# Optimization experiments

Measured on AMD Instinct MI355X. Metric: run time of the kernel, lower is better.

Reference implementation:

```python
import jax, jax.numpy as jnp
import numpy as np

EPS = 1e-5

def gather_neighbour(pc, idx):
    # pc: [B,N,d], idx: [B,Q,k] -> [B,Q,k,d]
    return jax.vmap(lambda p, i: p[i])(pc, idx)

def rel_pos_encoding(q_xyz, src_xyz, idx):
    # q_xyz: [B,Q,3], src_xyz: [B,N,3], idx: [B,Q,k] -> [B,Q,k,10]
    nbr = gather_neighbour(src_xyz, idx)              # [B,Q,k,3]
    tile = q_xyz[:, :, None, :]                       # [B,Q,1,3]
    rel = tile - nbr                                  # [B,Q,k,3]
    dis = jnp.sqrt(jnp.sum(rel * rel, axis=-1, keepdims=True))
    tile_b = jnp.broadcast_to(tile, nbr.shape)
    return jnp.concatenate([dis, rel, tile_b, nbr], axis=-1)

def conv_bn_relu(x, W, g, b, m, v):
    # 1x1 conv (bias-free) + inference BatchNorm + ReLU; x: [B,Q,K,Cin], W: [Cout,Cin]
    y = jnp.einsum('bqkc,oc->bqko', x, W)
    y = (y - m) * (g * jax.lax.rsqrt(v + EPS)) + b
    return jax.nn.relu(y)

def att_pool(x, Wfc, Wm, g, b, m, v):
    # x: [B,Q,K,C] -> [B,Q,1,Cout]; softmax over neighbor axis K
    att = jnp.einsum('bqkc,oc->bqko', x, Wfc)
    att = jax.nn.softmax(att, axis=2)
    agg = jnp.sum(x * att, axis=2, keepdims=True)     # [B,Q,1,C]
    return conv_bn_relu(agg, Wm, g, b, m, v)

def setup_inputs() -> dict:
    key = jax.random.key(0)
    ks = jax.random.split(key, 40)
    B, Q, k, Nd, Ns = 2, 16384, 16, 4096, 16384
    dim_lb, dim_sc, dim_nl = 128, 64, 128
    d_mid = dim_lb + 10 - dim_sc   # 74
    d_att = dim_lb + 10            # 138
    f32 = jnp.float32
    inp = {}
    inp['features_lb'] = jax.random.normal(ks[0], (B, Q, k, dim_lb), f32)
    inp['features_sc'] = jax.random.normal(ks[1], (B, Q, k, dim_sc), f32)
    inp['NM_lb'] = jax.random.randint(ks[2], (B, Q, k), 0, Nd)
    inp['NM_sc'] = jax.random.randint(ks[3], (B, Q, k), 0, Ns)
    inp['coords_lb'] = jax.random.normal(ks[4], (B, Nd, 3), f32)
    inp['coords_sc'] = jax.random.normal(ks[5], (B, Ns, 3), f32)
    inp['coords_queries'] = jax.random.normal(ks[6], (B, Q, 3), f32)
    inp['NM_cl'] = jax.random.randint(ks[7], (B, Q, k), 0, Q)
    def bn(i, c):
        return (jax.random.uniform(ks[i], (c,), f32) + 0.5,
                jax.random.normal(ks[i + 1], (c,), f32) * 0.1,
                jax.random.normal(ks[i + 2], (c,), f32) * 0.1,
                jax.random.uniform(ks[i + 3], (c,), f32) + 0.5)
    inp['W_lb'] = jax.random.normal(ks[8], (10, 10), f32) * 0.3
    inp['g_lb'], inp['b_lb'], inp['m_lb'], inp['v_lb'] = bn(9, 10)
    inp['W_sc'] = jax.random.normal(ks[13], (d_mid, 10), f32) * 0.3
    inp['g_sc'], inp['b_sc'], inp['m_sc'], inp['v_sc'] = bn(14, d_mid)
    inp['W_fc1'] = jax.random.normal(ks[18], (d_att, d_att), f32) * 0.08
    inp['W_mlp1'] = jax.random.normal(ks[19], (dim_nl, d_att), f32) * 0.08
    inp['g1'], inp['b1'], inp['m1'], inp['v1'] = bn(20, dim_nl)
    inp['W_cl'] = jax.random.normal(ks[24], (10, 10), f32) * 0.3
    inp['g_cl'], inp['b_cl'], inp['m_cl'], inp['v_cl'] = bn(25, 10)
    inp['W_fc2'] = jax.random.normal(ks[29], (d_att, d_att), f32) * 0.08
    inp['W_mlp2'] = jax.random.normal(ks[30], (dim_nl, d_att), f32) * 0.08
    inp['g2'], inp['b2'], inp['m2'], inp['v2'] = bn(31, dim_nl)
    return inp

def reference(features_lb, features_sc, NM_lb, NM_sc, coords_lb, coords_sc,
              coords_queries, NM_cl,
              W_lb, g_lb, b_lb, m_lb, v_lb,
              W_sc, g_sc, b_sc, m_sc, v_sc,
              W_fc1, W_mlp1, g1, b1, m1, v1,
              W_cl, g_cl, b_cl, m_cl, v_cl,
              W_fc2, W_mlp2, g2, b2, m2, v2):
    # branch 1: layer-below
    rppe_lb = conv_bn_relu(rel_pos_encoding(coords_queries, coords_lb, NM_lb),
                           W_lb, g_lb, b_lb, m_lb, v_lb)          # [B,Q,k,10]
    # branch 2: skip connection
    rppe_sc = conv_bn_relu(rel_pos_encoding(coords_queries, coords_sc, NM_sc),
                           W_sc, g_sc, b_sc, m_sc, v_sc)          # [B,Q,k,74]
    locSE_lb = jnp.concatenate([rppe_lb, features_lb], axis=-1)   # [B,Q,k,138]
    locSE_sc = jnp.concatenate([rppe_sc, features_sc], axis=-1)   # [B,Q,k,138]
    f_hat = jnp.concatenate([locSE_lb, locSE_sc], axis=2)         # [B,Q,2k,138]
    f_tilde = att_pool(f_hat, W_fc1, W_mlp1, g1, b1, m1, v1)      # [B,Q,1,128]
    # second aggregation over current layer (num_agg > 1)
    rppe_cl = conv_bn_relu(rel_pos_encoding(coords_queries, coords_queries, NM_cl),
                           W_cl, g_cl, b_cl, m_cl, v_cl)          # [B,Q,k,10]
    f_cur = gather_neighbour(f_tilde[:, :, 0, :], NM_cl)          # [B,Q,k,128]
    locSE_cl = jnp.concatenate([rppe_cl, f_cur], axis=-1)         # [B,Q,k,138]
    f_tilde = att_pool(locSE_cl, W_fc2, W_mlp2, g2, b2, m2, v2)   # [B,Q,1,128]
    # match torch output layout [B, dim_nl, Q, 1]
    return jnp.transpose(f_tilde, (0, 3, 1, 2))
```

## Files before the change

kernel.cpp:

```cpp
#include <hip/hip_runtime.h>
#include <cmath>

#define EPSF 1e-5f
typedef unsigned int  uint32;
typedef unsigned short u16;
typedef __attribute__((ext_vector_type(8))) short bfrag;
typedef __attribute__((ext_vector_type(4))) float f32x4;

constexpr int Qn   = 16384;
constexpr int KS   = 168;
constexpr int PXS  = 42;
constexpr int AGS  = 168;
constexpr int Nd   = 4096;
constexpr float LOG2E = 1.4426950408889634f;

constexpr int OFF_W1  = 0;
constexpr int OFF_WM1 = 23040;
constexpr int OFF_W2  = 43520;
constexpr int OFF_WM2 = 66560;
constexpr int OFF_WLB = 87040;
constexpr int OFF_WSC = 87552;
constexpr int OFF_WCL = 90112;
constexpr int END_W   = 90624;
constexpr int BN_LB = 0;
constexpr int BN_SC = 20;
constexpr int BN_CL = 168;
constexpr int BN_M1 = 188;
constexpr int BN_M2 = 444;
constexpr int BN_TOT = 700;
constexpr int OFF_FT  = END_W + 2 * BN_TOT;
constexpr int PREP_N  = END_W + BN_TOT;

__device__ __forceinline__ u16 f2b(float f) {
    uint32 u = __float_as_uint(f);
    uint32 r = (u + 0x7fffu + ((u >> 16) & 1u)) >> 16;
    return (u16)r;
}
__device__ __forceinline__ float b2f(u16 h) {
    return __uint_as_float(((uint32)h) << 16);
}
__device__ __forceinline__ uint32 cvtpk(float a, float b) {
    uint32 r;
    asm("v_cvt_pk_bf16_f32 %0, %1, %2" : "=v"(r) : "v"(a), "v"(b));
    return r;
}
__device__ __forceinline__ u16 cvt1(float a) { return (u16)cvtpk(a, a); }
__device__ __forceinline__ float exp2_hw(float x) { return __builtin_amdgcn_exp2f(x); }

__global__ __launch_bounds__(256) void prep_weights(
    const float* __restrict__ Wfc1, const float* __restrict__ Wmlp1,
    const float* __restrict__ Wfc2, const float* __restrict__ Wmlp2,
    const float* __restrict__ Wlb,  const float* __restrict__ Wsc,
    const float* __restrict__ Wcl,
    const float* __restrict__ g_lb, const float* __restrict__ b_lb,
    const float* __restrict__ m_lb, const float* __restrict__ v_lb,
    const float* __restrict__ g_sc, const float* __restrict__ b_sc,
    const float* __restrict__ m_sc, const float* __restrict__ v_sc,
    const float* __restrict__ g_cl, const float* __restrict__ b_cl,
    const float* __restrict__ m_cl, const float* __restrict__ v_cl,
    const float* __restrict__ g1, const float* __restrict__ b1,
    const float* __restrict__ m1, const float* __restrict__ v1,
    const float* __restrict__ g2, const float* __restrict__ b2,
    const float* __restrict__ m2, const float* __restrict__ v2,
    u16* __restrict__ ws16)
{
    int i = blockIdx.x * 256 + threadIdx.x;
    if (i >= PREP_N) return;
    if (i >= END_W) {
        int j = i - END_W;
        const float *g, *bb, *m, *v; int o2;
        if (j < BN_SC)      { g = g_lb; bb = b_lb; m = m_lb; v = v_lb; o2 = j - BN_LB; }
        else if (j < BN_CL) { g = g_sc; bb = b_sc; m = m_sc; v = v_sc; o2 = j - BN_SC; }
        else if (j < BN_M1) { g = g_cl; bb = b_cl; m = m_cl; v = v_cl; o2 = j - BN_CL; }
        else if (j < BN_M2) { g = g1;   bb = b1;   m = m1;   v = v1;   o2 = j - BN_M1; }
        else                { g = g2;   bb = b2;   m = m2;   v = v2;   o2 = j - BN_M2; }
        int o = o2 >> 1;
        float sc_ = g[o] * rsqrtf(v[o] + EPSF);
        ((float*)(ws16 + END_W))[j] = (o2 & 1) ? (bb[o] - m[o] * sc_) : sc_;
        return;
    }
    int lane = (i >> 3) & 63, jj = i & 7;
    int row16 = lane & 15;
    int kf = ((lane >> 4) << 3) + jj;
    float v = 0.f;
    if (i < OFF_WLB) {
        const float* src; int nrows; int idx; bool fc = false;
        if (i < OFF_WM1)      { src = Wfc1;  nrows = 138; idx = i - OFF_W1;  fc = true; }
        else if (i < OFF_W2)  { src = Wmlp1; nrows = 128; idx = i - OFF_WM1; }
        else if (i < OFF_WM2) { src = Wfc2;  nrows = 138; idx = i - OFF_W2;  fc = true; }
        else                  { src = Wmlp2; nrows = 128; idx = i - OFF_WM2; }
        int t = idx >> 9, nt = t / 5, kt = t - nt * 5;
        int row = nt * 16 + row16;
        int kp  = kt * 32 + kf;
        int k   = (kp < 10) ? kp : kp - 2;
        if (row < nrows && kp < 140 && kp != 10 && kp != 11) {
            v = src[row * 138 + k];
            if (fc) v *= LOG2E;
        }
    } else {
        const float* src; int nrows; int idx;
        if (i < OFF_WSC)      { src = Wlb; nrows = 10; idx = i - OFF_WLB; }
        else if (i < OFF_WCL) { src = Wsc; nrows = 74; idx = i - OFF_WSC; }
        else                  { src = Wcl; nrows = 10; idx = i - OFF_WCL; }
        int t = idx >> 9;
        int row = t * 16 + row16;
        if (row < nrows && kf < 10) v = src[row * 10 + kf];
    }
    ws16[i] = f2b(v);
}

__device__ __forceinline__ void loadB(bfrag (&bf)[5], const u16* __restrict__ Wt,
                                      int nt, int lane) {
    #pragma unroll
    for (int kt = 0; kt < 5; ++kt)
        bf[kt] = *(const bfrag*)&Wt[((nt * 5 + kt) << 9) + (lane << 3)];
}
__device__ __forceinline__ void mfma32(const bfrag (&af)[2][5], const bfrag (&bf)[5],
                                       f32x4 &a0, f32x4 &a1) {
    const f32x4 zf = {0.f, 0.f, 0.f, 0.f};
    a0 = zf; a1 = zf;
    #pragma unroll
    for (int kt = 0; kt < 5; ++kt) {
        a0 = __builtin_amdgcn_mfma_f32_16x16x32_bf16(af[0][kt], bf[kt], a0, 0, 0, 0);
        a1 = __builtin_amdgcn_mfma_f32_16x16x32_bf16(af[1][kt], bf[kt], a1, 0, 0, 0);
    }
}
__device__ __forceinline__ void mfma16(const bfrag (&af)[5], const bfrag (&bf)[5],
                                       f32x4 &a0) {
    const f32x4 zf = {0.f, 0.f, 0.f, 0.f};
    a0 = zf;
    #pragma unroll
    for (int kt = 0; kt < 5; ++kt)
        a0 = __builtin_amdgcn_mfma_f32_16x16x32_bf16(af[kt], bf[kt], a0, 0, 0, 0);
}
__device__ __forceinline__ void soft32(
    const f32x4& a0, const f32x4& a1, int nt,
    int lane, int lrow, const u16* __restrict__ fr0, const u16* __restrict__ fr1,
    u16* __restrict__ ag)
{
    const int ch  = nt * 16 + lrow;
    const int chp = ch + (ch >= 10 ? 2 : 0);
    float s = 0.f, num = 0.f;
    #pragma unroll
    for (int r = 0; r < 4; ++r) {
        float e = exp2_hw(a0[r]);
        s += e;
        num += e * b2f(fr0[r * KS + chp]);
    }
    #pragma unroll
    for (int r = 0; r < 4; ++r) {
        float e = exp2_hw(a1[r]);
        s += e;
        num += e * b2f(fr1[r * KS + chp]);
    }
    s   += __shfl_xor(s, 16);   s   += __shfl_xor(s, 32);
    num += __shfl_xor(num, 16); num += __shfl_xor(num, 32);
    if (lane < 16)
        ag[chp] = cvt1((ch < 138) ? num * __builtin_amdgcn_rcpf(s) : 0.f);
}
__device__ __forceinline__ void soft16(
    const f32x4& a0, int nt,
    int lane, int lrow, const u16* __restrict__ fr0, u16* __restrict__ ag)
{
    const int ch  = nt * 16 + lrow;
    const int chp = ch + (ch >= 10 ? 2 : 0);
    float s = 0.f, num = 0.f;
    #pragma unroll
    for (int r = 0; r < 4; ++r) {
        float e = exp2_hw(a0[r]);
        s += e;
        num += e * b2f(fr0[r * KS + chp]);
    }
    s   += __shfl_xor(s, 16);   s   += __shfl_xor(s, 32);
    num += __shfl_xor(num, 16); num += __shfl_xor(num, 32);
    if (lane < 16)
        ag[chp] = cvt1((ch < 138) ? num * __builtin_amdgcn_rcpf(s) : 0.f);
}
#define SB() __builtin_amdgcn_sched_barrier(0)

__global__ __launch_bounds__(256, 4) void stage1(
    const float* __restrict__ feat_lb, const float* __restrict__ feat_sc,
    const int* __restrict__ nm_lb, const int* __restrict__ nm_sc,
    const float* __restrict__ c_lb, const float* __restrict__ c_sc,
    const float* __restrict__ c_q,
    u16* __restrict__ ws16)
{
    __shared__ __align__(16) u16 fhat[64 * KS];
    __shared__ __align__(16) u16 pxs[64 * PXS];
    u16* aggs = pxs;

    const int tid  = threadIdx.x;
    const int bq0  = blockIdx.x * 2;
    const int b    = bq0 >> 14;
    const int lane = tid & 63;
    const int w    = tid >> 6;
    const int lrow = lane & 15;
    const int lgr  = lane >> 4;
    const int q    = w >> 1;
    const int h    = w & 1;

    const u16* W1t  = ws16 + OFF_W1;
    const u16* Wm1t = ws16 + OFF_WM1;
    const float* bn = (const float*)(ws16 + END_W);
    u16* ft = ws16 + OFF_FT;

    bfrag wcv[3];
    float2 bnv[3];
    if (h == 0) {
        wcv[0] = *(const bfrag*)&ws16[OFF_WLB + (lane << 3)];
        wcv[1] = *(const bfrag*)&ws16[OFF_WSC + (lane << 3)];
        wcv[2] = *(const bfrag*)&ws16[OFF_WSC + 512 + (lane << 3)];
        bnv[0] = (lrow < 10) ? *(const float2*)&bn[BN_LB + lrow * 2] : float2{0.f, 0.f};
        bnv[1] = *(const float2*)&bn[BN_SC + lrow * 2];
        bnv[2] = *(const float2*)&bn[BN_SC + (16 + lrow) * 2];
    } else {
        #pragma unroll
        for (int t = 0; t < 3; ++t) {
            wcv[t] = *(const bfrag*)&ws16[OFF_WSC + ((2 + t) << 9) + (lane << 3)];
            int o = (2 + t) * 16 + lrow;
            bnv[t] = (o < 74) ? *(const float2*)&bn[BN_SC + o * 2] : float2{0.f, 0.f};
        }
    }

    {
        const float4* flb = (const float4*)(feat_lb + (size_t)bq0 * 2048);
        float4 r0[4];
        #pragma unroll
        for (int it = 0; it < 4; ++it) r0[it] = flb[tid + it * 256];
        const float4* fsc = (const float4*)(feat_sc + (size_t)bq0 * 1024);
        float4 r1[2];
        #pragma unroll
        for (int it = 0; it < 2; ++it) r1[it] = fsc[tid + it * 256];
        #pragma unroll
        for (int it = 0; it < 4; ++it) {
            int u = tid + it * 256;
            int qq = u >> 9, rem = u & 511, r = rem >> 5, c4 = rem & 31;
            uint32* d = (uint32*)&fhat[(qq * 32 + r) * KS + 12 + c4 * 4];
            d[0] = cvtpk(r0[it].x, r0[it].y); d[1] = cvtpk(r0[it].z, r0[it].w);
        }
        #pragma unroll
        for (int it = 0; it < 2; ++it) {
            int u = tid + it * 256;
            int qq = u >> 8, rem = u & 255, r = rem >> 4, c4 = rem & 15;
            uint32* d = (uint32*)&fhat[(qq * 32 + 16 + r) * KS + 76 + c4 * 4];
            d[0] = cvtpk(r1[it].x, r1[it].y); d[1] = cvtpk(r1[it].z, r1[it].w);
        }
        for (int u = tid; u < 64 * 15; u += 256) {
            int row = u / 15, jj = u - row * 15;
            uint32* base = (uint32*)((char*)fhat + row * 336);
            if (jj == 0) base[5] = 0u; else base[69 + jj] = 0u;
        }
    }
    if (tid < 64) {
        const int qq = tid >> 5, r = tid & 31;
        const int bq = bq0 + qq;
        const bool lb = r < 16;
        const int idx = lb ? nm_lb[bq * 16 + r] : nm_sc[bq * 16 + (r - 16)];
        const float* nb = lb ? (c_lb + ((size_t)b * Nd + idx) * 3)
                             : (c_sc + ((size_t)b * Qn + idx) * 3);
        const float qx = c_q[bq * 3 + 0], qy = c_q[bq * 3 + 1], qz = c_q[bq * 3 + 2];
        const float nx = nb[0], ny = nb[1], nz = nb[2];
        const float rx = qx - nx, ry = qy - ny, rz = qz - nz;
        const float dd = sqrtf(rx * rx + ry * ry + rz * rz);
        uint32* pw = (uint32*)&pxs[tid * PXS];
        pw[0] = cvtpk(dd, rx); pw[1] = cvtpk(ry, rz); pw[2] = cvtpk(qx, qy);
        pw[3] = cvtpk(qz, nx); pw[4] = cvtpk(ny, nz);
        #pragma unroll
        for (int z = 5; z < 16; ++z) pw[z] = 0u;
    }
    __syncthreads();

    const f32x4 zf = {0.f, 0.f, 0.f, 0.f};

    {
        bfrag pa1 = *(const bfrag*)&pxs[(q * 32 + 16 + lrow) * PXS + lgr * 8];
        if (h == 0) {
            bfrag pa0 = *(const bfrag*)&pxs[(q * 32 + lrow) * PXS + lgr * 8];
            f32x4 c = __builtin_amdgcn_mfma_f32_16x16x32_bf16(pa0, wcv[0], zf, 0, 0, 0);
            if (lrow < 10) {
                #pragma unroll
                for (int r = 0; r < 4; ++r)
                    fhat[(q * 32 + lgr * 4 + r) * KS + lrow] =
                        cvt1(fmaxf(c[r] * bnv[0].x + bnv[0].y, 0.f));
            }
            #pragma unroll
            for (int t = 1; t < 3; ++t) {
                f32x4 c2 = __builtin_amdgcn_mfma_f32_16x16x32_bf16(pa1, wcv[t], zf, 0, 0, 0);
                const int o  = (t - 1) * 16 + lrow;
                const int cp = (o < 10) ? o : o + 2;
                #pragma unroll
                for (int r = 0; r < 4; ++r)
                    fhat[(q * 32 + 16 + lgr * 4 + r) * KS + cp] =
                        cvt1(fmaxf(c2[r] * bnv[t].x + bnv[t].y, 0.f));
            }
        } else {
            #pragma unroll
            for (int t = 0; t < 3; ++t) {
                f32x4 c2 = __builtin_amdgcn_mfma_f32_16x16x32_bf16(pa1, wcv[t], zf, 0, 0, 0);
                const int o = (2 + t) * 16 + lrow;
                if (o < 74) {
                    #pragma unroll
                    for (int r = 0; r < 4; ++r)
                        fhat[(q * 32 + 16 + lgr * 4 + r) * KS + o + 2] =
                            cvt1(fmaxf(c2[r] * bnv[t].x + bnv[t].y, 0.f));
                }
            }
        }
    }
    __syncthreads();

    bfrag af[2][5];
    #pragma unroll
    for (int mt = 0; mt < 2; ++mt)
        #pragma unroll
        for (int kt = 0; kt < 5; ++kt)
            af[mt][kt] = *(const bfrag*)&fhat[(q * 32 + mt * 16 + lrow) * KS + kt * 32 + lgr * 8];

    const u16* fr0 = fhat + (q * 32 + lgr * 4) * KS;
    const u16* fr1 = fr0 + 16 * KS;
    u16* ag = aggs + q * AGS;

    bfrag b0[5], b1[5];
    f32x4 a0, a1;
    if (h == 0) {
        loadB(b0, W1t, 0, lane);
        loadB(b1, W1t, 1, lane); mfma32(af, b0, a0, a1); SB(); soft32(a0, a1, 0, lane, lrow, fr0, fr1, ag);
        loadB(b0, W1t, 2, lane); mfma32(af, b1, a0, a1); SB(); soft32(a0, a1, 1, lane, lrow, fr0, fr1, ag);
        loadB(b1, W1t, 3, lane); mfma32(af, b0, a0, a1); SB(); soft32(a0, a1, 2, lane, lrow, fr0, fr1, ag);
        loadB(b0, W1t, 4, lane); mfma32(af, b1, a0, a1); SB(); soft32(a0, a1, 3, lane, lrow, fr0, fr1, ag);
        mfma32(af, b0, a0, a1); soft32(a0, a1, 4, lane, lrow, fr0, fr1, ag);
        if (lane < 2)       ag[10 + lane] = 0;
        else if (lane < 16) ag[144 + lane] = 0;
    } else {
        loadB(b0, W1t, 5, lane);
        loadB(b1, W1t, 6, lane); mfma32(af, b0, a0, a1); SB(); soft32(a0, a1, 5, lane, lrow, fr0, fr1, ag);
        loadB(b0, W1t, 7, lane); mfma32(af, b1, a0, a1); SB(); soft32(a0, a1, 6, lane, lrow, fr0, fr1, ag);
        loadB(b1, W1t, 8, lane); mfma32(af, b0, a0, a1); SB(); soft32(a0, a1, 7, lane, lrow, fr0, fr1, ag);
        mfma32(af, b1, a0, a1); soft32(a0, a1, 8, lane, lrow, fr0, fr1, ag);
    }
    __syncthreads();

    bfrag am[5];
    #pragma unroll
    for (int kt = 0; kt < 5; ++kt)
        am[kt] = *(const bfrag*)&aggs[lrow * AGS + kt * 32 + lgr * 8];
    #pragma unroll
    for (int oi = 0; oi < 2; ++oi) {
        const int ot = w * 2 + oi;
        f32x4 c = zf;
        #pragma unroll
        for (int kt = 0; kt < 5; ++kt) {
            bfrag wm = *(const bfrag*)&Wm1t[(((ot * 5) + kt) << 9) + (lane << 3)];
            c = __builtin_amdgcn_mfma_f32_16x16x32_bf16(am[kt], wm, c, 0, 0, 0);
        }
        if (lgr == 0) {
            const int o = ot * 16 + lrow;
            float2 p = *(const float2*)&bn[BN_M1 + o * 2];
            #pragma unroll
            for (int r = 0; r < 2; ++r)
                ft[(size_t)(bq0 + r) * 128 + o] = cvt1(fmaxf(c[r] * p.x + p.y, 0.f));
        }
    }
}

__global__ __launch_bounds__(512, 4) void stage2(
    const int* __restrict__ nm_cl, const float* __restrict__ c_q,
    const u16* __restrict__ ws16, float* __restrict__ out)
{
    __shared__ __align__(16) u16 fhat[128 * KS];
    __shared__ __align__(16) u16 pxs[128 * PXS];
    u16* aggs = pxs;

    const int tid  = threadIdx.x;
    const int bq0  = blockIdx.x * 8;
    const int b    = bq0 >> 14;
    const int q0   = bq0 & (Qn - 1);
    const int lane = tid & 63;
    const int w    = tid >> 6;
    const int lrow = lane & 15;
    const int lgr  = lane >> 4;

    const u16* W2t  = ws16 + OFF_W2;
    const u16* Wm2t = ws16 + OFF_WM2;
    const float* bn = (const float*)(ws16 + END_W);
    const u16* ft   = ws16 + OFF_FT;

    bfrag wcl = *(const bfrag*)&ws16[OFF_WCL + (lane << 3)];
    float2 bncl = (lrow < 10) ? *(const float2*)&bn[BN_CL + lrow * 2] : float2{0.f, 0.f};

    for (int u = tid; u < 128 * 15; u += 512) {
        int row = u / 15, jj = u - row * 15;
        uint32* base = (uint32*)((char*)fhat + row * 336);
        if (jj == 0) base[5] = 0u; else base[69 + jj] = 0u;
    }
    if (tid < 128) {
        const int qq = tid >> 4, r = tid & 15;
        const int bq = bq0 + qq;
        const int idx = nm_cl[bq * 16 + r];
        const float* nb = c_q + ((size_t)(b << 14) + idx) * 3;
        const float qx = c_q[bq * 3 + 0], qy = c_q[bq * 3 + 1], qz = c_q[bq * 3 + 2];
        const float nx = nb[0], ny = nb[1], nz = nb[2];
        const float rx = qx - nx, ry = qy - ny, rz = qz - nz;
        const float dd = sqrtf(rx * rx + ry * ry + rz * rz);
        uint32* pw = (uint32*)&pxs[tid * PXS];
        pw[0] = cvtpk(dd, rx); pw[1] = cvtpk(ry, rz); pw[2] = cvtpk(qx, qy);
        pw[3] = cvtpk(qz, nx); pw[4] = cvtpk(ny, nz);
        #pragma unroll
        for (int z = 5; z < 16; ++z) pw[z] = 0u;
    }
    #pragma unroll
    for (int i = 0; i < 16; ++i) {
        int u = tid + i * 512;
        int row = u >> 6, c2 = u & 63;
        int qq = row >> 4;
        int idx = nm_cl[(bq0 + qq) * 16 + (row & 15)];
        const uint32* srow = (const uint32*)(ft + (size_t)((b << 14) + idx) * 128);
        *(uint32*)&fhat[row * KS + 12 + c2 * 2] = srow[c2];
    }
    __syncthreads();

    const f32x4 zf = {0.f, 0.f, 0.f, 0.f};

    {
        bfrag pa = *(const bfrag*)&pxs[(w * 16 + lrow) * PXS + lgr * 8];
        f32x4 c = __builtin_amdgcn_mfma_f32_16x16x32_bf16(pa, wcl, zf, 0, 0, 0);
        if (lrow < 10) {
            #pragma unroll
            for (int r = 0; r < 4; ++r)
                fhat[(w * 16 + lgr * 4 + r) * KS + lrow] =
                    cvt1(fmaxf(c[r] * bncl.x + bncl.y, 0.f));
        }
    }
    __syncthreads();

    bfrag af[5];
    #pragma unroll
    for (int kt = 0; kt < 5; ++kt)
        af[kt] = *(const bfrag*)&fhat[(w * 16 + lrow) * KS + kt * 32 + lgr * 8];

    const u16* fr0 = fhat + (w * 16 + lgr * 4) * KS;
    u16* ag = aggs + w * AGS;

    bfrag b0[5], b1[5];
    f32x4 a0;
    loadB(b0, W2t, 0, lane);
    loadB(b1, W2t, 1, lane); mfma16(af, b0, a0); SB(); soft16(a0, 0, lane, lrow, fr0, ag);
    loadB(b0, W2t, 2, lane); mfma16(af, b1, a0); SB(); soft16(a0, 1, lane, lrow, fr0, ag);
    loadB(b1, W2t, 3, lane); mfma16(af, b0, a0); SB(); soft16(a0, 2, lane, lrow, fr0, ag);
    loadB(b0, W2t, 4, lane); mfma16(af, b1, a0); SB(); soft16(a0, 3, lane, lrow, fr0, ag);
    loadB(b1, W2t, 5, lane); mfma16(af, b0, a0); SB(); soft16(a0, 4, lane, lrow, fr0, ag);
    loadB(b0, W2t, 6, lane); mfma16(af, b1, a0); SB(); soft16(a0, 5, lane, lrow, fr0, ag);
    loadB(b1, W2t, 7, lane); mfma16(af, b0, a0); SB(); soft16(a0, 6, lane, lrow, fr0, ag);
    loadB(b0, W2t, 8, lane); mfma16(af, b1, a0); SB(); soft16(a0, 7, lane, lrow, fr0, ag);
    mfma16(af, b0, a0); soft16(a0, 8, lane, lrow, fr0, ag);
    if (lane < 2)       ag[10 + lane] = 0;
    else if (lane < 16) ag[144 + lane] = 0;
    __syncthreads();

    bfrag am[5];
    #pragma unroll
    for (int kt = 0; kt < 5; ++kt)
        am[kt] = *(const bfrag*)&aggs[lrow * AGS + kt * 32 + lgr * 8];
    {
        f32x4 c = zf;
        #pragma unroll
        for (int kt = 0; kt < 5; ++kt) {
            bfrag wm = *(const bfrag*)&Wm2t[(((w * 5) + kt) << 9) + (lane << 3)];
            c = __builtin_amdgcn_mfma_f32_16x16x32_bf16(am[kt], wm, c, 0, 0, 0);
        }
        if (lgr < 2) {
            const int o = w * 16 + lrow;
            float2 p = *(const float2*)&bn[BN_M2 + o * 2];
            #pragma unroll
            for (int r = 0; r < 4; ++r) {
                const int qloc = lgr * 4 + r;
                out[((size_t)(b * 128 + o) << 14) + q0 + qloc] = fmaxf(c[r] * p.x + p.y, 0.f);
            }
        }
    }
}

extern "C" void kernel_launch(void* const* d_in, const int* in_sizes, int n_in,
                              void* d_out, int out_size, void* d_ws, size_t ws_size,
                              hipStream_t stream)
{
    const float* feat_lb = (const float*)d_in[0];
    const float* feat_sc = (const float*)d_in[1];
    const int*   nm_lb   = (const int*)d_in[2];
    const int*   nm_sc   = (const int*)d_in[3];
    const float* c_lb    = (const float*)d_in[4];
    const float* c_sc    = (const float*)d_in[5];
    const float* c_q     = (const float*)d_in[6];
    const int*   nm_cl   = (const int*)d_in[7];
    const float* W_lb = (const float*)d_in[8];
    const float* g_lb = (const float*)d_in[9];
    const float* b_lb = (const float*)d_in[10];
    const float* m_lb = (const float*)d_in[11];
    const float* v_lb = (const float*)d_in[12];
    const float* W_sc = (const float*)d_in[13];
    const float* g_sc = (const float*)d_in[14];
    const float* b_sc = (const float*)d_in[15];
    const float* m_sc = (const float*)d_in[16];
    const float* v_sc = (const float*)d_in[17];
    const float* W_fc1  = (const float*)d_in[18];
    const float* W_mlp1 = (const float*)d_in[19];
    const float* g1 = (const float*)d_in[20];
    const float* b1 = (const float*)d_in[21];
    const float* m1 = (const float*)d_in[22];
    const float* v1 = (const float*)d_in[23];
    const float* W_cl = (const float*)d_in[24];
    const float* g_cl = (const float*)d_in[25];
    const float* b_cl = (const float*)d_in[26];
    const float* m_cl = (const float*)d_in[27];
    const float* v_cl = (const float*)d_in[28];
    const float* W_fc2  = (const float*)d_in[29];
    const float* W_mlp2 = (const float*)d_in[30];
    const float* g2 = (const float*)d_in[31];
    const float* b2 = (const float*)d_in[32];
    const float* m2 = (const float*)d_in[33];
    const float* v2 = (const float*)d_in[34];

    u16* ws16 = (u16*)d_ws;
    float* out = (float*)d_out;

    hipLaunchKernelGGL(prep_weights, dim3((PREP_N + 255) / 256), dim3(256), 0, stream,
        W_fc1, W_mlp1, W_fc2, W_mlp2, W_lb, W_sc, W_cl,
        g_lb, b_lb, m_lb, v_lb, g_sc, b_sc, m_sc, v_sc,
        g_cl, b_cl, m_cl, v_cl, g1, b1, m1, v1, g2, b2, m2, v2, ws16);

    hipLaunchKernelGGL(stage1, dim3(2 * Qn / 2), dim3(256), 0, stream,
        feat_lb, feat_sc, nm_lb, nm_sc, c_lb, c_sc, c_q, ws16);

    hipLaunchKernelGGL(stage2, dim3(2 * Qn / 8), dim3(512), 0, stream,
        nm_cl, c_q, ws16, out);
}
```

Before: 225.3 us.

## Split attention pooling and MLP into separate kernels with per-query blocks

Both stages now run one query per block of two waves and write the softmax-aggregated vectors to a global workspace. Separate mlp1/mlp2 kernels then do the 138→128 projections as dense 16-row MFMA tiles. Before, each block's MLP used mostly-padded M rows (2 or 8 queries in a 16-row tile). This removes that wasted MFMA work and the in-block barrier, at the cost of two extra launches and an aggregate round trip through global memory. Stage2 also splits its nine softmax output tiles across two waves.

```diff
diff --git a/kernel.cpp b/kernel.cpp
--- a/kernel.cpp
+++ b/kernel.cpp
@@ -29,6 +29,7 @@
 constexpr int BN_M2 = 444;
 constexpr int BN_TOT = 700;
 constexpr int OFF_FT  = END_W + 2 * BN_TOT;
+constexpr int OFF_AG  = OFF_FT + 2 * Qn * 128;
 constexpr int PREP_N  = END_W + BN_TOT;
 
 __device__ __forceinline__ u16 f2b(float f) {
@@ -178,31 +179,27 @@
 }
 #define SB() __builtin_amdgcn_sched_barrier(0)
 
-__global__ __launch_bounds__(256, 4) void stage1(
+__global__ __launch_bounds__(128, 8) void stage1(
     const float* __restrict__ feat_lb, const float* __restrict__ feat_sc,
     const int* __restrict__ nm_lb, const int* __restrict__ nm_sc,
     const float* __restrict__ c_lb, const float* __restrict__ c_sc,
     const float* __restrict__ c_q,
     u16* __restrict__ ws16)
 {
-    __shared__ __align__(16) u16 fhat[64 * KS];
-    __shared__ __align__(16) u16 pxs[64 * PXS];
-    u16* aggs = pxs;
+    __shared__ __align__(16) u16 fhat[32 * KS];
+    __shared__ __align__(16) u16 pxs[32 * PXS];
 
     const int tid  = threadIdx.x;
-    const int bq0  = blockIdx.x * 2;
-    const int b    = bq0 >> 14;
+    const int bq   = blockIdx.x;
+    const int b    = bq >> 14;
     const int lane = tid & 63;
-    const int w    = tid >> 6;
+    const int h    = tid >> 6;
     const int lrow = lane & 15;
     const int lgr  = lane >> 4;
-    const int q    = w >> 1;
-    const int h    = w & 1;
 
     const u16* W1t  = ws16 + OFF_W1;
-    const u16* Wm1t = ws16 + OFF_WM1;
     const float* bn = (const float*)(ws16 + END_W);
-    u16* ft = ws16 + OFF_FT;
+    u16* ag = ws16 + OFF_AG + (size_t)bq * AGS;
 
     bfrag wcv[3];
     float2 bnv[3];
@@ -223,37 +220,40 @@
     }
 
     {
-        const float4* flb = (const float4*)(feat_lb + (size_t)bq0 * 2048);
+        const float4* flb = (const float4*)(feat_lb + (size_t)bq * 2048);
         float4 r0[4];
         #pragma unroll
-        for (int it = 0; it < 4; ++it) r0[it] = flb[tid + it * 256];
-        const float4* fsc = (const float4*)(feat_sc + (size_t)bq0 * 1024);
+        for (int it = 0; it < 4; ++it) r0[it] = flb[tid + it * 128];
+        const float4* fsc = (const float4*)(feat_sc + (size_t)bq * 1024);
         float4 r1[2];
         #pragma unroll
-        for (int it = 0; it < 2; ++it) r1[it] = fsc[tid + it * 256];
+        for (int it = 0; it < 2; ++it) r1[it] = fsc[tid + it * 128];
         #pragma unroll
         for (int it = 0; it < 4; ++it) {
-            int u = tid + it * 256;
-            int qq = u >> 9, rem = u & 511, r = rem >> 5, c4 = rem & 31;
-            uint32* d = (uint32*)&fhat[(qq * 32 + r) * KS + 12 + c4 * 4];
+            int u = tid + it * 128;
+            int nbr = u >> 5, c4 = u & 31;
+            uint32* d = (uint32*)&fhat[nbr * KS + 12 + c4 * 4];
             d[0] = cvtpk(r0[it].x, r0[it].y); d[1] = cvtpk(r0[it].z, r0[it].w);
         }
         #pragma unroll
         for (int it = 0; it < 2; ++it) {
-            int u = tid + it * 256;
-            int qq = u >> 8, rem = u & 255, r = rem >> 4, c4 = rem & 15;
-            uint32* d = (uint32*)&fhat[(qq * 32 + 16 + r) * KS + 76 + c4 * 4];
+            int u = tid + it * 128;
+            int nbr = u >> 4, c4 = u & 15;
+            uint32* d = (uint32*)&fhat[(16 + nbr) * KS + 76 + c4 * 4];
             d[0] = cvtpk(r1[it].x, r1[it].y); d[1] = cvtpk(r1[it].z, r1[it].w);
         }
-        for (int u = tid; u < 64 * 15; u += 256) {
-            int row = u / 15, jj = u - row * 15;
-            uint32* base = (uint32*)((char*)fhat + row * 336);
-            if (jj == 0) base[5] = 0u; else base[69 + jj] = 0u;
-        }
-    }
-    if (tid < 64) {
-        const int qq = tid >> 5, r = tid & 31;
-        const int bq = bq0 + qq;
+        if (tid < 32) ((uint32*)((char*)fhat + tid * 336))[5] = 0u;
+        #pragma unroll
+        for (int it = 0; it < 4; ++it) {
+            int u = tid + it * 128;
+            if (u < 448) {
+                int row = u / 14, jj = u - row * 14;
+                ((uint32*)((char*)fhat + row * 336))[70 + jj] = 0u;
+            }
+        }
+    }
+    if (tid < 32) {
+        const int r = tid;
         const bool lb = r < 16;
         const int idx = lb ? nm_lb[bq * 16 + r] : nm_sc[bq * 16 + (r - 16)];
         const float* nb = lb ? (c_lb + ((size_t)b * Nd + idx) * 3)
@@ -273,14 +273,14 @@
     const f32x4 zf = {0.f, 0.f, 0.f, 0.f};
 
     {
-        bfrag pa1 = *(const bfrag*)&pxs[(q * 32 + 16 + lrow) * PXS + lgr * 8];
+        bfrag pa1 = *(const bfrag*)&pxs[(16 + lrow) * PXS + lgr * 8];
         if (h == 0) {
-            bfrag pa0 = *(const bfrag*)&pxs[(q * 32 + lrow) * PXS + lgr * 8];
+            bfrag pa0 = *(const bfrag*)&pxs[lrow * PXS + lgr * 8];
             f32x4 c = __builtin_amdgcn_mfma_f32_16x16x32_bf16(pa0, wcv[0], zf, 0, 0, 0);
             if (lrow < 10) {
                 #pragma unroll
                 for (int r = 0; r < 4; ++r)
-                    fhat[(q * 32 + lgr * 4 + r) * KS + lrow] =
+                    fhat[(lgr * 4 + r) * KS + lrow] =
                         cvt1(fmaxf(c[r] * bnv[0].x + bnv[0].y, 0.f));
             }
             #pragma unroll
@@ -290,7 +290,7 @@
                 const int cp = (o < 10) ? o : o + 2;
                 #pragma unroll
                 for (int r = 0; r < 4; ++r)
-                    fhat[(q * 32 + 16 + lgr * 4 + r) * KS + cp] =
+                    fhat[(16 + lgr * 4 + r) * KS + cp] =
                         cvt1(fmaxf(c2[r] * bnv[t].x + bnv[t].y, 0.f));
             }
         } else {
@@ -301,7 +301,7 @@
                 if (o < 74) {
                     #pragma unroll
                     for (int r = 0; r < 4; ++r)
-                        fhat[(q * 32 + 16 + lgr * 4 + r) * KS + o + 2] =
+                        fhat[(16 + lgr * 4 + r) * KS + o + 2] =
                             cvt1(fmaxf(c2[r] * bnv[t].x + bnv[t].y, 0.f));
                 }
             }
@@ -314,11 +314,10 @@
     for (int mt = 0; mt < 2; ++mt)
         #pragma unroll
         for (int kt = 0; kt < 5; ++kt)
-            af[mt][kt] = *(const bfrag*)&fhat[(q * 32 + mt * 16 + lrow) * KS + kt * 32 + lgr * 8];
-
-    const u16* fr0 = fhat + (q * 32 + lgr * 4) * KS;
+            af[mt][kt] = *(const bfrag*)&fhat[(mt * 16 + lrow) * KS + kt * 32 + lgr * 8];
+
+    const u16* fr0 = fhat + (lgr * 4) * KS;
     const u16* fr1 = fr0 + 16 * KS;
-    u16* ag = aggs + q * AGS;
 
     bfrag b0[5], b1[5];
     f32x4 a0, a1;
@@ -338,65 +337,42 @@
         loadB(b1, W1t, 8, lane); mfma32(af, b0, a0, a1); SB(); soft32(a0, a1, 7, lane, lrow, fr0, fr1, ag);
         mfma32(af, b1, a0, a1); soft32(a0, a1, 8, lane, lrow, fr0, fr1, ag);
     }
-    __syncthreads();
-
-    bfrag am[5];
-    #pragma unroll
-    for (int kt = 0; kt < 5; ++kt)
-        am[kt] = *(const bfrag*)&aggs[lrow * AGS + kt * 32 + lgr * 8];
-    #pragma unroll
-    for (int oi = 0; oi < 2; ++oi) {
-        const int ot = w * 2 + oi;
-        f32x4 c = zf;
-        #pragma unroll
-        for (int kt = 0; kt < 5; ++kt) {
-            bfrag wm = *(const bfrag*)&Wm1t[(((ot * 5) + kt) << 9) + (lane << 3)];
-            c = __builtin_amdgcn_mfma_f32_16x16x32_bf16(am[kt], wm, c, 0, 0, 0);
-        }
-        if (lgr == 0) {
-            const int o = ot * 16 + lrow;
-            float2 p = *(const float2*)&bn[BN_M1 + o * 2];
-            #pragma unroll
-            for (int r = 0; r < 2; ++r)
-                ft[(size_t)(bq0 + r) * 128 + o] = cvt1(fmaxf(c[r] * p.x + p.y, 0.f));
-        }
-    }
-}
-
-__global__ __launch_bounds__(512, 4) void stage2(
+}
+
+__global__ __launch_bounds__(128, 8) void stage2a(
     const int* __restrict__ nm_cl, const float* __restrict__ c_q,
-    const u16* __restrict__ ws16, float* __restrict__ out)
-{
-    __shared__ __align__(16) u16 fhat[128 * KS];
-    __shared__ __align__(16) u16 pxs[128 * PXS];
-    u16* aggs = pxs;
+    u16* __restrict__ ws16)
+{
+    __shared__ __align__(16) u16 fhat[16 * KS];
+    __shared__ __align__(16) u16 pxs[16 * PXS];
 
     const int tid  = threadIdx.x;
-    const int bq0  = blockIdx.x * 8;
-    const int b    = bq0 >> 14;
-    const int q0   = bq0 & (Qn - 1);
+    const int bq   = blockIdx.x;
+    const int b    = bq >> 14;
     const int lane = tid & 63;
-    const int w    = tid >> 6;
+    const int h    = tid >> 6;
     const int lrow = lane & 15;
     const int lgr  = lane >> 4;
 
     const u16* W2t  = ws16 + OFF_W2;
-    const u16* Wm2t = ws16 + OFF_WM2;
     const float* bn = (const float*)(ws16 + END_W);
     const u16* ft   = ws16 + OFF_FT;
+    u16* ag = ws16 + OFF_AG + (size_t)bq * AGS;
 
     bfrag wcl = *(const bfrag*)&ws16[OFF_WCL + (lane << 3)];
     float2 bncl = (lrow < 10) ? *(const float2*)&bn[BN_CL + lrow * 2] : float2{0.f, 0.f};
 
-    for (int u = tid; u < 128 * 15; u += 512) {
-        int row = u / 15, jj = u - row * 15;
-        uint32* base = (uint32*)((char*)fhat + row * 336);
-        if (jj == 0) base[5] = 0u; else base[69 + jj] = 0u;
-    }
-    if (tid < 128) {
-        const int qq = tid >> 4, r = tid & 15;
-        const int bq = bq0 + qq;
-        const int idx = nm_cl[bq * 16 + r];
+    if (tid < 16) ((uint32*)((char*)fhat + tid * 336))[5] = 0u;
+    #pragma unroll
+    for (int it = 0; it < 2; ++it) {
+        int u = tid + it * 128;
+        if (u < 224) {
+            int row = u / 14, jj = u - row * 14;
+            ((uint32*)((char*)fhat + row * 336))[70 + jj] = 0u;
+        }
+    }
+    if (tid < 16) {
+        const int idx = nm_cl[bq * 16 + tid];
         const float* nb = c_q + ((size_t)(b << 14) + idx) * 3;
         const float qx = c_q[bq * 3 + 0], qy = c_q[bq * 3 + 1], qz = c_q[bq * 3 + 2];
         const float nx = nb[0], ny = nb[1], nz = nb[2];
@@ -409,11 +385,10 @@
         for (int z = 5; z < 16; ++z) pw[z] = 0u;
     }
     #pragma unroll
-    for (int i = 0; i < 16; ++i) {
-        int u = tid + i * 512;
+    for (int it = 0; it < 8; ++it) {
+        int u = tid + it * 128;
         int row = u >> 6, c2 = u & 63;
-        int qq = row >> 4;
-        int idx = nm_cl[(bq0 + qq) * 16 + (row & 15)];
+        int idx = nm_cl[bq * 16 + row];
         const uint32* srow = (const uint32*)(ft + (size_t)((b << 14) + idx) * 128);
         *(uint32*)&fhat[row * KS + 12 + c2 * 2] = srow[c2];
     }
@@ -421,13 +396,13 @@
 
     const f32x4 zf = {0.f, 0.f, 0.f, 0.f};
 
-    {
-        bfrag pa = *(const bfrag*)&pxs[(w * 16 + lrow) * PXS + lgr * 8];
+    if (h == 0) {
+        bfrag pa = *(const bfrag*)&pxs[lrow * PXS + lgr * 8];
         f32x4 c = __builtin_amdgcn_mfma_f32_16x16x32_bf16(pa, wcl, zf, 0, 0, 0);
         if (lrow < 10) {
             #pragma unroll
             for (int r = 0; r < 4; ++r)
-                fhat[(w * 16 + lgr * 4 + r) * KS + lrow] =
+                fhat[(lgr * 4 + r) * KS + lrow] =
                     cvt1(fmaxf(c[r] * bncl.x + bncl.y, 0.f));
         }
     }
@@ -436,46 +411,104 @@
     bfrag af[5];
     #pragma unroll
     for (int kt = 0; kt < 5; ++kt)
-        af[kt] = *(const bfrag*)&fhat[(w * 16 + lrow) * KS + kt * 32 + lgr * 8];
-
-    const u16* fr0 = fhat + (w * 16 + lgr * 4) * KS;
-    u16* ag = aggs + w * AGS;
+        af[kt] = *(const bfrag*)&fhat[lrow * KS + kt * 32 + lgr * 8];
+
+    const u16* fr0 = fhat + (lgr * 4) * KS;
 
     bfrag b0[5], b1[5];
     f32x4 a0;
-    loadB(b0, W2t, 0, lane);
-    loadB(b1, W2t, 1, lane); mfma16(af, b0, a0); SB(); soft16(a0, 0, lane, lrow, fr0, ag);
-    loadB(b0, W2t, 2, lane); mfma16(af, b1, a0); SB(); soft16(a0, 1, lane, lrow, fr0, ag);
-    loadB(b1, W2t, 3, lane); mfma16(af, b0, a0); SB(); soft16(a0, 2, lane, lrow, fr0, ag);
-    loadB(b0, W2t, 4, lane); mfma16(af, b1, a0); SB(); soft16(a0, 3, lane, lrow, fr0, ag);
-    loadB(b1, W2t, 5, lane); mfma16(af, b0, a0); SB(); soft16(a0, 4, lane, lrow, fr0, ag);
-    loadB(b0, W2t, 6, lane); mfma16(af, b1, a0); SB(); soft16(a0, 5, lane, lrow, fr0, ag);
-    loadB(b1, W2t, 7, lane); mfma16(af, b0, a0); SB(); soft16(a0, 6, lane, lrow, fr0, ag);
-    loadB(b0, W2t, 8, lane); mfma16(af, b1, a0); SB(); soft16(a0, 7, lane, lrow, fr0, ag);
-    mfma16(af, b0, a0); soft16(a0, 8, lane, lrow, fr0, ag);
-    if (lane < 2)       ag[10 + lane] = 0;
-    else if (lane < 16) ag[144 + lane] = 0;
-    __syncthreads();
-
-    bfrag am[5];
+    if (h == 0) {
+        loadB(b0, W2t, 0, lane);
+        loadB(b1, W2t, 1, lane); mfma16(af, b0, a0); SB(); soft16(a0, 0, lane, lrow, fr0, ag);
+        loadB(b0, W2t, 2, lane); mfma16(af, b1, a0); SB(); soft16(a0, 1, lane, lrow, fr0, ag);
+        loadB(b1, W2t, 3, lane); mfma16(af, b0, a0); SB(); soft16(a0, 2, lane, lrow, fr0, ag);
+        mfma16(af, b1, a0); soft16(a0, 3, lane, lrow, fr0, ag);
+        loadB(b0, W2t, 4, lane); mfma16(af, b0, a0); soft16(a0, 4, lane, lrow, fr0, ag);
+        if (lane < 2)       ag[10 + lane] = 0;
+        else if (lane < 16) ag[144 + lane] = 0;
+    } else {
+        loadB(b0, W2t, 5, lane);
+        loadB(b1, W2t, 6, lane); mfma16(af, b0, a0); SB(); soft16(a0, 5, lane, lrow, fr0, ag);
+        loadB(b0, W2t, 7, lane); mfma16(af, b1, a0); SB(); soft16(a0, 6, lane, lrow, fr0, ag);
+        loadB(b1, W2t, 8, lane); mfma16(af, b0, a0); SB(); soft16(a0, 7, lane, lrow, fr0, ag);
+        mfma16(af, b1, a0); soft16(a0, 8, lane, lrow, fr0, ag);
+    }
+}
+
+__global__ __launch_bounds__(256) void mlp1(const u16* __restrict__ ws16,
+                                            u16* __restrict__ ws16w)
+{
+    const int tid  = threadIdx.x;
+    const int lane = tid & 63;
+    const int w    = tid >> 6;
+    const int lrow = lane & 15;
+    const int lgr  = lane >> 4;
+    const int q0   = (blockIdx.x * 4 + w) * 16;
+
+    const u16* Wm = ws16 + OFF_WM1;
+    const float* bn = (const float*)(ws16 + END_W);
+    const u16* agg = ws16 + OFF_AG;
+    u16* ftg = ws16w + OFF_FT;
+
+    bfrag af[5];
     #pragma unroll
     for (int kt = 0; kt < 5; ++kt)
-        am[kt] = *(const bfrag*)&aggs[lrow * AGS + kt * 32 + lgr * 8];
-    {
+        af[kt] = *(const bfrag*)&agg[(size_t)(q0 + lrow) * AGS + kt * 32 + lgr * 8];
+
+    const f32x4 zf = {0.f, 0.f, 0.f, 0.f};
+    #pragma unroll
+    for (int ot = 0; ot < 8; ++ot) {
+        bfrag bf[5];
+        loadB(bf, Wm, ot, lane);
         f32x4 c = zf;
         #pragma unroll
-        for (int kt = 0; kt < 5; ++kt) {
-            bfrag wm = *(const bfrag*)&Wm2t[(((w * 5) + kt) << 9) + (lane << 3)];
-            c = __builtin_amdgcn_mfma_f32_16x16x32_bf16(am[kt], wm, c, 0, 0, 0);
-        }
-        if (lgr < 2) {
-            const int o = w * 16 + lrow;
-            float2 p = *(const float2*)&bn[BN_M2 + o * 2];
-            #pragma unroll
-            for (int r = 0; r < 4; ++r) {
-                const int qloc = lgr * 4 + r;
-                out[((size_t)(b * 128 + o) << 14) + q0 + qloc] = fmaxf(c[r] * p.x + p.y, 0.f);
-            }
+        for (int kt = 0; kt < 5; ++kt)
+            c = __builtin_amdgcn_mfma_f32_16x16x32_bf16(af[kt], bf[kt], c, 0, 0, 0);
+        const int o = ot * 16 + lrow;
+        float2 p = *(const float2*)&bn[BN_M1 + o * 2];
+        #pragma unroll
+        for (int r = 0; r < 4; ++r) {
+            int q = q0 + lgr * 4 + r;
+            ftg[(size_t)q * 128 + o] = cvt1(fmaxf(c[r] * p.x + p.y, 0.f));
+        }
+    }
+}
+
+__global__ __launch_bounds__(256) void mlp2(const u16* __restrict__ ws16,
+                                            float* __restrict__ out)
+{
+    const int tid  = threadIdx.x;
+    const int lane = tid & 63;
+    const int w    = tid >> 6;
+    const int lrow = lane & 15;
+    const int lgr  = lane >> 4;
+    const int q0   = (blockIdx.x * 4 + w) * 16;
+
+    const u16* Wm = ws16 + OFF_WM2;
+    const float* bn = (const float*)(ws16 + END_W);
+    const u16* agg = ws16 + OFF_AG;
+
+    bfrag af[5];
+    #pragma unroll
+    for (int kt = 0; kt < 5; ++kt)
+        af[kt] = *(const bfrag*)&agg[(size_t)(q0 + lrow) * AGS + kt * 32 + lgr * 8];
+
+    const f32x4 zf = {0.f, 0.f, 0.f, 0.f};
+    #pragma unroll
+    for (int ot = 0; ot < 8; ++ot) {
+        bfrag bf[5];
+        loadB(bf, Wm, ot, lane);
+        f32x4 c = zf;
+        #pragma unroll
+        for (int kt = 0; kt < 5; ++kt)
+            c = __builtin_amdgcn_mfma_f32_16x16x32_bf16(af[kt], bf[kt], c, 0, 0, 0);
+        const int o = ot * 16 + lrow;
+        float2 p = *(const float2*)&bn[BN_M2 + o * 2];
+        #pragma unroll
+        for (int r = 0; r < 4; ++r) {
+            int q = q0 + lgr * 4 + r;
+            int bb = q >> 14, qq = q & (Qn - 1);
+            out[((size_t)(bb * 128 + o) << 14) + qq] = fmaxf(c[r] * p.x + p.y, 0.f);
         }
     }
 }
@@ -528,9 +561,13 @@
         g_lb, b_lb, m_lb, v_lb, g_sc, b_sc, m_sc, v_sc,
         g_cl, b_cl, m_cl, v_cl, g1, b1, m1, v1, g2, b2, m2, v2, ws16);
 
-    hipLaunchKernelGGL(stage1, dim3(2 * Qn / 2), dim3(256), 0, stream,
+    hipLaunchKernelGGL(stage1, dim3(2 * Qn), dim3(128), 0, stream,
         feat_lb, feat_sc, nm_lb, nm_sc, c_lb, c_sc, c_q, ws16);
 
-    hipLaunchKernelGGL(stage2, dim3(2 * Qn / 8), dim3(512), 0, stream,
-        nm_cl, c_q, ws16, out);
-}
+    hipLaunchKernelGGL(mlp1, dim3(2 * Qn / 64), dim3(256), 0, stream, ws16, ws16);
+
+    hipLaunchKernelGGL(stage2a, dim3(2 * Qn), dim3(128), 0, stream,
+        nm_cl, c_q, ws16);
+
+    hipLaunchKernelGGL(mlp2, dim3(2 * Qn / 64), dim3(256), 0, stream, ws16, out);
+}
```

New measurement: 227.7 us. Within noise of the previous version (+1.1%).
